# Optimization experiments

Hardware: AMD Instinct MI355X
Metric: run time of the kernel (lower is better)

The kernel has to match this reference:

```python
import jax, jax.numpy as jnp
import numpy as np

LAMBDA_SOFTMAX = 20.0  # opt.lambda_softmax
EPS = 1e-8
NEG = -1e30


def l2norm(x, axis):
    # torch l2norm: x / (sqrt(sum x^2) + eps)
    n = jnp.sqrt(jnp.sum(x * x, axis=axis, keepdims=True)) + EPS
    return x / n


def cosine(x1, x2, axis):
    # torch compute_similarity: sum(x1*x2)/clamp(|x1||x2|, min=eps)
    w12 = jnp.sum(x1 * x2, axis=axis)
    w1 = jnp.sqrt(jnp.sum(x1 * x1, axis=axis))
    w2 = jnp.sqrt(jnp.sum(x2 * x2, axis=axis))
    return w12 / jnp.maximum(w1 * w2, EPS)


def _focal_renorm(a, sourceL):
    # focal_equal: fattn = 1[a*S - sum(a) > 0], then renormalize fattn*a
    funcF = a * sourceL - jnp.sum(a, axis=-1, keepdims=True)
    fattn = jnp.where(funcF > 0, 1.0, 0.0)
    ta = fattn * a
    s = jnp.sum(ta, axis=-1, keepdims=True)
    return ta / jnp.where(s > 0, s, 1.0)


def compute_weiTexts(img_q, img_v, txt_k_all, txt_v_all, text_length):
    N, R, d = img_q.shape          # n_img, n_region, d
    Lw = txt_k_all.shape[1]        # max words
    qn_img = l2norm(img_q, -1)     # [N,R,d]
    mask_all = (jnp.arange(Lw)[None, :] < text_length[:, None])  # [T,Lw] bool

    def per_text(txt_k, txt_v, mask, n_word):
        # mask out padded words (torch slices [:n_word])
        m = mask.astype(txt_k.dtype)[:, None]        # [Lw,1]
        tk = l2norm(txt_k * m, -1)                   # [Lw,d], padded rows -> 0
        tv = txt_v * m                                # [Lw,d]

        # ---- i2t: query=img, context=text (sourceL = n_word) ----
        attn = jnp.einsum('ld,nrd->nlr', tk, qn_img)  # bmm(key_norm, queryT) [N,Lw,R]
        attn = jax.nn.leaky_relu(attn, 0.1)
        attn = l2norm(attn, 2)                        # over R
        attn = jnp.transpose(attn, (0, 2, 1))         # [N,R,Lw]
        logits = jnp.where(mask[None, None, :], attn * LAMBDA_SOFTMAX, NEG)
        a = jax.nn.softmax(logits, axis=-1)           # [N,R,Lw]
        a = _focal_renorm(a, n_word)
        wei_text = jnp.einsum('nrl,ld->nrd', a, tv)   # [N,R,d]
        wei_text = l2norm(wei_text, 2)
        i2t = jnp.mean(cosine(img_v, wei_text, 2), axis=1)  # [N]

        # ---- t2i: query=text, context=img (sourceL = R) ----
        attn2 = jnp.einsum('nrd,ld->nrl', qn_img, tk)  # bmm(key_norm, queryT) [N,R,Lw]
        attn2 = jax.nn.leaky_relu(attn2, 0.1)
        attn2 = l2norm(attn2, 2)                       # over Lw (padded cols are 0)
        attn2 = jnp.transpose(attn2, (0, 2, 1))        # [N,Lw,R]
        a2 = jax.nn.softmax(attn2 * LAMBDA_SOFTMAX, axis=-1)
        a2 = _focal_renorm(a2, float(R))
        wei_img = jnp.einsum('nlr,nrd->nld', a2, img_v)  # [N,Lw,d]
        wei_img = l2norm(wei_img, 2)
        cos2 = cosine(tv[None, :, :], wei_img, 2)        # [N,Lw]; padded rows -> 0
        t2i = jnp.sum(cos2 * mask.astype(cos2.dtype)[None, :], axis=1) / n_word
        return i2t, t2i

    n_word_f = text_length.astype(img_q.dtype)
    i2t_T, t2i_T = jax.vmap(per_text)(txt_k_all, txt_v_all, mask_all, n_word_f)
    # loop concatenated along dim 1 -> [n_img, n_txt]
    return i2t_T.T, t2i_T.T


def setup_inputs() -> dict:
    key = jax.random.key(0)
    k1, k2, k3, k4, k5 = jax.random.split(key, 5)
    N, T, R, Lw, d = 128, 128, 48, 64, 1024
    return {
        'local_img_query': jax.random.normal(k1, (N, R, d), dtype=jnp.float32),
        'local_img_value': jax.random.normal(k2, (N, R, d), dtype=jnp.float32),
        'local_text_key': jax.random.normal(k3, (T, Lw, d), dtype=jnp.float32),
        'local_text_value': jax.random.normal(k4, (T, Lw, d), dtype=jnp.float32),
        'text_length': jax.random.randint(k5, (T,), 16, Lw + 1, dtype=jnp.int32),
    }


def reference(local_img_query, local_img_value, local_text_key, local_text_value, text_length):
    return compute_weiTexts(local_img_query, local_img_value,
                            local_text_key, local_text_value, text_length)
```

## Files before the change

### kernel.cpp

```cpp
#include <hip/hip_runtime.h>

#define NIMG 128
#define NTXT 128
#define RDIM 48
#define LWRD 64
#define DDIM 1024
#define LAMB 20.0f
#define FEPS 1e-8f

#define WS_INVQ 0
#define WS_VN   6144
#define WS_INVK 12288
#define WS_TVN  20480
#define WS_H    28672
#define WS_VG   552960
#define WS_MID_BYTES 3391488ull
#define WS_HU   847872
#define WS_VGU  1372160
#define SP_TK   3334144
#define SP_TV   20111360
#define SP_Q    36888576
#define SP_V    49471488
#define WS_BIG_BYTES 124108800ull

typedef unsigned int u32;
typedef unsigned short u16;
typedef __attribute__((ext_vector_type(8))) short short8;
typedef __attribute__((ext_vector_type(4))) float f32x4;
typedef __attribute__((ext_vector_type(4))) u32 uintx4;
typedef __attribute__((ext_vector_type(2))) u32 uintx2;

#define MFMA(a,b,c) __builtin_amdgcn_mfma_f32_16x16x32_bf16(a,b,c,0,0,0)

__device__ __forceinline__ u32 f2bf(float x){
    u32 u = __float_as_uint(x);
    return (u + 0x7fffu + ((u >> 16) & 1u)) >> 16;
}
__device__ __forceinline__ float bf2f(u32 h){ return __uint_as_float(h << 16); }
__device__ __forceinline__ u32 packsplit(float x){
    u32 h = f2bf(x);
    u32 l = f2bf(x - bf2f(h));
    return h | (l << 16);
}
__device__ __forceinline__ void unpk(uintx4 a, uintx4 b, short8& hi, short8& lo){
    uintx4 h, l;
    h.x = (a.x & 0xffffu) | (a.y << 16);
    h.y = (a.z & 0xffffu) | (a.w << 16);
    h.z = (b.x & 0xffffu) | (b.y << 16);
    h.w = (b.z & 0xffffu) | (b.w << 16);
    l.x = (a.x >> 16) | (a.y & 0xffff0000u);
    l.y = (a.z >> 16) | (a.w & 0xffff0000u);
    l.z = (b.x >> 16) | (b.y & 0xffff0000u);
    l.w = (b.z >> 16) | (b.w & 0xffff0000u);
    hi = __builtin_bit_cast(short8, h);
    lo = __builtin_bit_cast(short8, l);
}

#define PSTR  40
#define PTKH  0
#define PTVH  2560
#define PQH   5120
#define PVH   8960
#define LOGAP 12800
__device__ __forceinline__ void split_store(short* stg, int idx, float4 x, float sc){
    float a0 = x.x*sc, a1 = x.y*sc, a2 = x.z*sc, a3 = x.w*sc;
    u32 h0=f2bf(a0), h1=f2bf(a1), h2=f2bf(a2), h3=f2bf(a3);
    u32 l0=f2bf(a0-bf2f(h0)), l1=f2bf(a1-bf2f(h1)), l2=f2bf(a2-bf2f(h2)), l3=f2bf(a3-bf2f(h3));
    uintx2 hv; hv.x = h0 | (h1<<16); hv.y = h2 | (h3<<16);
    uintx2 lv; lv.x = l0 | (l1<<16); lv.y = l2 | (l3<<16);
    *(uintx2*)(stg + idx)         = hv;
    *(uintx2*)(stg + idx + LOGAP) = lv;
}
__device__ __forceinline__ short8 frag_ld(const short* stg, int plane, int rb, int m16, int quad){
    return *(const short8*)(stg + plane + (rb + m16) * PSTR + quad * 8);
}

__global__ __launch_bounds__(256, 2)
void prep_norms(const float* __restrict__ imq, const float* __restrict__ imv,
                const float* __restrict__ txk, const float* __restrict__ txv,
                float* __restrict__ ws) {
    int vid = blockIdx.x * 4 + (threadIdx.x >> 6);
    int lane = threadIdx.x & 63;
    const float* src;
    if (vid < 6144)       src = imq + (size_t)vid * 1024;
    else if (vid < 12288) src = imv + (size_t)(vid - 6144) * 1024;
    else if (vid < 20480) src = txk + (size_t)(vid - 12288) * 1024;
    else                  src = txv + (size_t)(vid - 20480) * 1024;
    const float4* s4 = (const float4*)src;
    float acc = 0.f;
#pragma unroll
    for (int j = 0; j < 4; ++j) {
        float4 v = s4[lane + 64 * j];
        acc += v.x * v.x + v.y * v.y + v.z * v.z + v.w * v.w;
    }
#pragma unroll
    for (int off = 32; off; off >>= 1) acc += __shfl_down(acc, off, 64);
    if (lane == 0) {
        float nrm = sqrtf(acc);
        if (vid < 6144)       ws[vid] = 1.f / (nrm + FEPS);
        else if (vid < 12288) ws[vid] = nrm;
        else if (vid < 20480) ws[vid] = 1.f / (nrm + FEPS);
        else                  ws[vid] = nrm;
    }
}

__global__ __launch_bounds__(256, 2)
void split_kernel(const float* __restrict__ imq, const float* __restrict__ imv,
                  const float* __restrict__ txk, const float* __restrict__ txv,
                  const int* __restrict__ tlen, const float* __restrict__ wsf,
// ... 22 lines not shown
        sc = (ten == 2) ? wsf[WS_INVQ + slab * 48 + row] : 1.f;
        dst = (size_t)(ten == 2 ? SP_Q : SP_V) + (size_t)slab * 98304
            + kc * 1536 + row * 32 + ks * 8;
        psz = 49152;
    }
    float4 x0 = *(const float4*)src;
    float4 x1 = *(const float4*)(src + 4);
    float v[8] = {x0.x, x0.y, x0.z, x0.w, x1.x, x1.y, x1.z, x1.w};
    short8 hv, lv;
#pragma unroll
    for (int i = 0; i < 8; ++i) {
        float a = v[i] * sc;
        u32 h = f2bf(a);
        hv[i] = (short)h;
        lv[i] = (short)f2bf(a - bf2f(h));
    }
    *(short8*)(wss + dst) = hv;
    *(short8*)(wss + dst + psz) = lv;
}

template <int TS>
__device__ __forceinline__ void gram_body(const float* __restrict__ src,
                                          float* __restrict__ dstf,
                                          u32* __restrict__ dstu,
                                          int mode, int nw, float* sT){
    const int NR = TS * 16;
    int ar = threadIdx.x >> 4, ac = threadIdx.x & 15;
    float acc[TS][TS];
#pragma unroll
    for (int i = 0; i < TS; ++i)
#pragma unroll
        for (int j = 0; j < TS; ++j) acc[i][j] = 0.f;
    for (int kc = 0; kc < 8; ++kc) {
        int k0 = kc * 128;
        for (int jid = threadIdx.x; jid < NR * 32; jid += 256) {
            int row = jid >> 5, c4 = jid & 31;
            float4 x = *(const float4*)(src + row * 1024 + k0 + c4 * 4);
            float sc = (row < nw) ? 1.f : 0.f;
            x.x *= sc; x.y *= sc; x.z *= sc; x.w *= sc;
            *(float4*)&sT[row * 132 + c4 * 4] = x;
        }
        __syncthreads();
#pragma unroll 4
        for (int k4 = 0; k4 < 32; ++k4) {
            float4 av[TS], bv[TS];
#pragma unroll
            for (int i = 0; i < TS; ++i) av[i] = *(const float4*)&sT[(TS*ar + i) * 132 + k4 * 4];
#pragma unroll
            for (int j = 0; j < TS; ++j) bv[j] = *(const float4*)&sT[(TS*ac + j) * 132 + k4 * 4];
#pragma unroll
            for (int i = 0; i < TS; ++i)
#pragma unroll
                for (int j = 0; j < TS; ++j)
                    acc[i][j] += av[i].x*bv[j].x + av[i].y*bv[j].y + av[i].z*bv[j].z + av[i].w*bv[j].w;
        }
        __syncthreads();
    }
#pragma unroll
    for (int i = 0; i < TS; ++i)
#pragma unroll
        for (int j = 0; j < TS; ++j) {
            int idx = (TS*ar + i) * NR + TS*ac + j;
            if (mode) dstu[idx] = packsplit(acc[i][j]);
            else      dstf[idx] = acc[i][j];
        }
}

__global__ __launch_bounds__(256, 2)
void gram_kernel(const float* __restrict__ txv, const float* __restrict__ imv,
                 const int* __restrict__ tlen, float* __restrict__ ws, int mode){
    __shared__ __align__(16) float sT[64 * 132];
    int b = blockIdx.x;
    u32* wsu = (u32*)ws;
    if (b < 128) {
        gram_body<4>(txv + (size_t)b * 65536, ws + WS_H + (size_t)b * 4096,
                     wsu + WS_HU + (size_t)b * 4096, mode, tlen[b], sT);
    } else {
        int n = b - 128;
        gram_body<3>(imv + (size_t)n * 49152, ws + WS_VG + (size_t)n * 2304,
                     wsu + WS_VGU + (size_t)n * 2304, mode, 48, sT);
    }
}

struct AFr { short8 kh[2], kl[2], th[2], tl[2]; };

__device__ __forceinline__ void load_af(AFr& A, const short* tkh, const short* tkl,
                                        const short* tvh, const short* tvl,
                                        int off, int r0, int r1){
    A.kh[0] = *(const short8*)(tkh + off + r0);
    A.kh[1] = *(const short8*)(tkh + off + r1);
    A.kl[0] = *(const short8*)(tkl + off + r0);
    A.kl[1] = *(const short8*)(tkl + off + r1);
    A.th[0] = *(const short8*)(tvh + off + r0);
    A.th[1] = *(const short8*)(tvh + off + r1);
    A.tl[0] = *(const short8*)(tvl + off + r0);
    A.tl[1] = *(const short8*)(tvl + off + r1);
}

__device__ __forceinline__ void mfma_step(const AFr& A, const short* stg,
                                          int nl, int m16, int quad,
                                          f32x4 (&accS)[2][3], f32x4 (&accG)[2][3]){
#pragma unroll
    for (int j = 0; j < 3; ++j) {
        int o = (nl * 48 + 16 * j + m16) * 40 + quad * 8;
        short8 bqh = *(const short8*)(stg + o);
        short8 bql = *(const short8*)(stg + 3840 + o);
        short8 bvh = *(const short8*)(stg + 7680 + o);
        short8 bvl = *(const short8*)(stg + 11520 + o);
#pragma unroll
        for (int i = 0; i < 2; ++i) {
            accS[i][j] = MFMA(A.kh[i], bqh, accS[i][j]);
            accS[i][j] = MFMA(A.kh[i], bql, accS[i][j]);
            accS[i][j] = MFMA(A.kl[i], bqh, accS[i][j]);
            accG[i][j] = MFMA(A.th[i], bvh, accG[i][j]);
            accG[i][j] = MFMA(A.th[i], bvl, accG[i][j]);
            accG[i][j] = MFMA(A.tl[i], bvh, accG[i][j]);
        }
    }
}

__global__ __launch_bounds__(256, 2)
void loss_mfma2(const int* __restrict__ tlen, const float* __restrict__ ws,
                float* __restrict__ out) {
    const int npair = blockIdx.x;
    const int t     = blockIdx.y;
    const int n0    = npair * 2;
    const int tid   = threadIdx.x;
    const int lane  = tid & 63;
    const int w     = tid >> 6;
    const int nl    = w >> 1;
    const int hh    = w & 1;
    const int quad  = lane >> 4;
    const int m16   = lane & 15;

    __shared__ __align__(16) float Sm[19776];
    short* stg   = (short*)Sm;
    u32*   A1w   = (u32*)Sm;
    u32*   A2w   = ((u32*)Sm) + 6528;
    float* P     = Sm + 12672;
    u32*   HVw   = (u32*)(Sm + 12672);
    float* sNl   = Sm + 19104;
    float* sNr   = Sm + 19232;
    float* sD1   = Sm + 19328;
    float* sS1   = Sm + 19424;
    float* sD2   = Sm + 19520;
    float* sS2   = Sm + 19648;

    const int nw = tlen[t];
    const float nwf = (float)nw;
    const short* wss = (const short*)ws;
    const u32*   wsu = (const u32*)ws;

    const short* bsrc[6]; int bdst[6];
#pragma unroll
    for (int it = 0; it < 6; ++it) {
        int jid = tid + 256 * it;
        int p = jid / 384; int rr = jid - p * 384;
        int row = rr >> 2, ks = rr & 3;
        int img = row >= 48; int grow = row - 48 * img;
        bsrc[it] = wss + (p < 2 ? SP_Q : SP_V) + (size_t)(n0 + img) * 98304
                 + (size_t)(p & 1) * 49152 + grow * 32 + ks * 8;
        bdst[it] = p * 3840 + row * 40 + ks * 8;
    }

    const short* tkh = wss + SP_TK + (size_t)t * 131072;
    const short* tkl = tkh + 65536;
    const short* tvh = wss + SP_TV + (size_t)t * 131072;
    const short* tvl = tvh + 65536;
    const int ar0 = (32 * hh + m16) * 32 + quad * 8;
    const int ar1 = ar0 + 512;

    f32x4 accS[2][3], accG[2][3];
    f32x4 zf = {0.f, 0.f, 0.f, 0.f};
#pragma unroll
    for (int i = 0; i < 2; ++i)
#pragma unroll
        for (int j = 0; j < 3; ++j) { accS[i][j] = zf; accG[i][j] = zf; }

    short8 bj[6];
#pragma unroll
    for (int it = 0; it < 6; ++it) bj[it] = *(const short8*)(bsrc[it]);
    AFr Ae, Ao;
    load_af(Ae, tkh, tkl, tvh, tvl, 0, ar0, ar1);

    for (int kc2 = 0; kc2 < 16; ++kc2) {
        const int kc = kc2 * 2;
        {
#pragma unroll
            for (int it = 0; it < 6; ++it) *(short8*)(stg + bdst[it]) = bj[it];
            __syncthreads();
            int bo = (kc + 1) * 1536;
#pragma unroll
            for (int it = 0; it < 6; ++it) bj[it] = *(const short8*)(bsrc[it] + bo);
            load_af(Ao, tkh, tkl, tvh, tvl, (kc + 1) * 2048, ar0, ar1);
            mfma_step(Ae, stg, nl, m16, quad, accS, accG);
            __syncthreads();
        }
        {
#pragma unroll
            for (int it = 0; it < 6; ++it) *(short8*)(stg + bdst[it]) = bj[it];
            __syncthreads();
            if (kc2 < 15) {
                int bo = (kc + 2) * 1536;
#pragma unroll
                for (int it = 0; it < 6; ++it) bj[it] = *(const short8*)(bsrc[it] + bo);
                load_af(Ae, tkh, tkl, tvh, tvl, (kc + 2) * 2048, ar0, ar1);
            }
            mfma_step(Ao, stg, nl, m16, quad, accS, accG);
            __syncthreads();
        }
    }

#pragma unroll
    for (int i = 0; i < 2; ++i)
#pragma unroll
        for (int j = 0; j < 3; ++j)
#pragma unroll
            for (int v = 0; v < 4; ++v) {
                int l = 32 * hh + 16 * i + quad * 4 + v;
                int r = 16 * j + m16;
                float x = accS[i][j][v];
                P[nl * 3136 + l * 49 + r] = (x > 0.f) ? x : 0.1f * x;
            }
    __syncthreads();

    if (tid < 128) {
        int n = tid >> 6, l = tid & 63;
        float s = 0.f;
#pragma unroll 4
        for (int r = 0; r < 48; ++r) { float x = P[n*3136 + l*49 + r]; s += x * x; }
        sNl[n * 64 + l] = sqrtf(s) + FEPS;
    } else if (tid < 224) {
        int i = tid - 128; int n = i >= 48; int r = i - 48 * n;
        float s = 0.f;
#pragma unroll 4
        for (int l = 0; l < 64; ++l) { float x = P[n*3136 + l*49 + r]; s += x * x; }
        sNr[n * 48 + r] = sqrtf(s) + FEPS;
    } else {
        for (int k = tid - 224; k < 448; k += 32) sD1[k] = 0.f;
    }
    __syncthreads();

    if (tid < 128) {
        int n = tid >> 6, l = tid & 63;
        u32* row = A2w + n * 3072 + l * 48;
        if (l < nw) {
            float a[48]; float mx = -1e30f;
            const float* Pr = P + n * 3136 + l * 49;
#pragma unroll
            for (int r = 0; r < 48; ++r) {
                float x = LAMB * Pr[r] / sNr[n * 48 + r];
                a[r] = x; mx = fmaxf(mx, x);
            }
            float se = 0.f;
#pragma unroll
            for (int r = 0; r < 48; ++r) { float e = __expf(a[r] - mx); a[r] = e; se += e; }
            float suma = 0.f;
#pragma unroll
            for (int r = 0; r < 48; ++r) { float x = a[r] / se; a[r] = x; suma += x; }
            float s2 = 0.f;
#pragma unroll
            for (int r = 0; r < 48; ++r) if (a[r] * 48.f - suma > 0.f) s2 += a[r];
            float ri = (s2 > 0.f) ? 1.f / s2 : 1.f;
#pragma unroll
            for (int r = 0; r < 48; ++r) {
                float x = (a[r] * 48.f - suma > 0.f) ? a[r] * ri : 0.f;
                row[r] = packsplit(x);
            }
        } else {
#pragma unroll
            for (int r = 0; r < 48; ++r) row[r] = 0u;
        }
    } else if (tid < 224) {
        int i = tid - 128; int n = i >= 48; int r = i - 48 * n;
        float a[64]; float mx = -1e30f;
#pragma unroll
        for (int l = 0; l < 64; ++l) {
            float x = (l < nw) ? (LAMB * P[n*3136 + l*49 + r] / sNl[n * 64 + l]) : -1e30f;
            a[l] = x; mx = fmaxf(mx, x);
        }
        float se = 0.f;
#pragma unroll
        for (int l = 0; l < 64; ++l) { float e = __expf(a[l] - mx); a[l] = e; se += e; }
        float suma = 0.f;
#pragma unroll
        for (int l = 0; l < 64; ++l) { float x = a[l] / se; a[l] = x; suma += x; }
        float s2 = 0.f;
#pragma unroll
        for (int l = 0; l < 64; ++l) if (a[l] * nwf - suma > 0.f) s2 += a[l];
        float ri = (s2 > 0.f) ? 1.f / s2 : 1.f;
        u32* row = A1w + n * 3264 + r * 68;
#pragma unroll
        for (int l = 0; l < 64; ++l) {
            float x = (a[l] * nwf - suma > 0.f) ? a[l] * ri : 0.f;
            row[l] = packsplit(x);
        }
    }
    __syncthreads();

    {
        const u32* Hg = wsu + WS_HU + (size_t)t * 4096;
        for (int jid = tid; jid < 1024; jid += 256) {
            int row = jid >> 4, c = jid & 15;
            *(uintx4*)&HVw[row * 68 + c * 4] = *(const uintx4*)&Hg[row * 64 + c * 4];
        }
    }
    __syncthreads();

    f32x4 accY[2][3];
    f32x4 zf2 = {0.f, 0.f, 0.f, 0.f};
#pragma unroll
    for (int i = 0; i < 2; ++i)
#pragma unroll
        for (int j = 0; j < 3; ++j) accY[i][j] = zf2;
#pragma unroll
    for (int ks = 0; ks < 2; ++ks) {
        int kb = ks * 32 + quad * 8;
        short8 Ah[2], Al[2];
#pragma unroll
        for (int i = 0; i < 2; ++i) {
            int row = 32 * hh + 16 * i + m16;
            uintx4 wa = *(const uintx4*)&HVw[row * 68 + kb];
            uintx4 wb = *(const uintx4*)&HVw[row * 68 + kb + 4];
            unpk(wa, wb, Ah[i], Al[i]);
        }
        short8 Bh[3], Bl[3];
#pragma unroll
        for (int j = 0; j < 3; ++j) {
            int base = nl * 3264 + (16 * j + m16) * 68 + kb;
            uintx4 wa = *(const uintx4*)&A1w[base];
            uintx4 wb = *(const uintx4*)&A1w[base + 4];
            unpk(wa, wb, Bh[j], Bl[j]);
        }
#pragma unroll
        for (int i = 0; i < 2; ++i)
#pragma unroll
            for (int j = 0; j < 3; ++j) {
                accY[i][j] = MFMA(Ah[i], Bh[j], accY[i][j]);
                accY[i][j] = MFMA(Ah[i], Bl[j], accY[i][j]);
                accY[i][j] = MFMA(Al[i], Bh[j], accY[i][j]);
            }
    }
    {
        float td[3] = {0.f, 0.f, 0.f}, ts[3] = {0.f, 0.f, 0.f};
#pragma unroll
        for (int i = 0; i < 2; ++i)
#pragma unroll
            for (int v = 0; v < 4; ++v) {
                int l = 32 * hh + 16 * i + quad * 4 + v;
#pragma unroll
                for (int j = 0; j < 3; ++j) {
                    u32 wv = A1w[nl * 3264 + (16 * j + m16) * 68 + l];
                    float av = bf2f(wv & 0xffffu) + bf2f(wv >> 16);
                    td[j] += av * accG[i][j][v];
                    ts[j] += av * accY[i][j][v];
                }
            }
#pragma unroll
        for (int j = 0; j < 3; ++j) {
            float d = td[j]; d += __shfl_xor(d, 16, 64); d += __shfl_xor(d, 32, 64);
            float s = ts[j]; s += __shfl_xor(s, 16, 64); s += __shfl_xor(s, 32, 64);
            if (quad == 0) {
                atomicAdd(&sD1[nl * 48 + 16 * j + m16], d);
                atomicAdd(&sS1[nl * 48 + 16 * j + m16], s);
            }
        }
    }
    __syncthreads();

    {
        const u32* Vgg = wsu + WS_VGU + (size_t)n0 * 2304;
        for (int jid = tid; jid < 1152; jid += 256) {
            int img = jid >= 576; int j2 = jid - 576 * img;
            int row = j2 / 12, c = j2 - row * 12;
            *(uintx4*)&HVw[img * 2496 + row * 52 + c * 4] =
                *(const uintx4*)&Vgg[(size_t)img * 2304 + row * 48 + c * 4];
        }
    }
    __syncthreads();

    f32x4 accY2[3][2];
#pragma unroll
    for (int i = 0; i < 3; ++i)
#pragma unroll
        for (int j = 0; j < 2; ++j) accY2[i][j] = zf2;
    const u32* VgW = HVw + nl * 2496;
#pragma unroll
    for (int ks = 0; ks < 2; ++ks) {
        const bool dead = (ks == 1) && (quad >= 2);
        const int kb = (ks == 0) ? quad * 8 : 32 + (quad & 1) * 8;
        short8 Ah2[3], Al2[3];
#pragma unroll
        for (int i = 0; i < 3; ++i) {
            uintx4 wa = {0,0,0,0}, wb = {0,0,0,0};
            if (!dead) {
                int row = 16 * i + m16;
                wa = *(const uintx4*)&VgW[row * 52 + kb];
                wb = *(const uintx4*)&VgW[row * 52 + kb + 4];
            }
            unpk(wa, wb, Ah2[i], Al2[i]);
        }
        short8 Bh2[2], Bl2[2];
#pragma unroll
        for (int j = 0; j < 2; ++j) {
            uintx4 wa = {0,0,0,0}, wb = {0,0,0,0};
            if (!dead) {
                int l = 32 * hh + 16 * j + m16;
                wa = *(const uintx4*)&A2w[nl * 3072 + l * 48 + kb];
                wb = *(const uintx4*)&A2w[nl * 3072 + l * 48 + kb + 4];
            }
            unpk(wa, wb, Bh2[j], Bl2[j]);
        }
#pragma unroll
        for (int i = 0; i < 3; ++i)
#pragma unroll
            for (int j = 0; j < 2; ++j) {
                accY2[i][j] = MFMA(Ah2[i], Bh2[j], accY2[i][j]);
                accY2[i][j] = MFMA(Ah2[i], Bl2[j], accY2[i][j]);
                accY2[i][j] = MFMA(Al2[i], Bh2[j], accY2[i][j]);
            }
    }
    {
        float u[2] = {0.f, 0.f};
#pragma unroll
        for (int i = 0; i < 3; ++i)
#pragma unroll
            for (int v = 0; v < 4; ++v) {
                int r = 16 * i + quad * 4 + v;
#pragma unroll
                for (int j = 0; j < 2; ++j) {
                    int l = 32 * hh + 16 * j + m16;
                    u32 wv = A2w[nl * 3072 + l * 48 + r];
                    float av = bf2f(wv & 0xffffu) + bf2f(wv >> 16);
                    u[j] += av * accY2[i][j][v];
                }
            }
#pragma unroll
        for (int j = 0; j < 2; ++j) {
            float s = u[j]; s += __shfl_xor(s, 16, 64); s += __shfl_xor(s, 32, 64);
            if (quad == 0) sS2[nl * 64 + 32 * hh + 16 * j + m16] = s;
        }
        float ud[2][4];
#pragma unroll
        for (int i = 0; i < 2; ++i)
#pragma unroll
            for (int v = 0; v < 4; ++v) ud[i][v] = 0.f;
#pragma unroll
        for (int i = 0; i < 2; ++i)
#pragma unroll
            for (int v = 0; v < 4; ++v) {
                int l = 32 * hh + 16 * i + quad * 4 + v;
#pragma unroll
                for (int j = 0; j < 3; ++j) {
                    u32 wv = A2w[nl * 3072 + l * 48 + (16 * j + m16)];
                    float av = bf2f(wv & 0xffffu) + bf2f(wv >> 16);
                    ud[i][v] += av * accG[i][j][v];
                }
            }
#pragma unroll
        for (int i = 0; i < 2; ++i)
#pragma unroll
            for (int v = 0; v < 4; ++v) {
                float d = ud[i][v];
                d += __shfl_xor(d, 1, 64); d += __shfl_xor(d, 2, 64);
                d += __shfl_xor(d, 4, 64); d += __shfl_xor(d, 8, 64);
                if (m16 == 0) sD2[nl * 64 + 32 * hh + 16 * i + quad * 4 + v] = d;
            }
    }
    __syncthreads();

    if (tid < 96) {
        int n = tid >= 48; int r = tid - 48 * n;
        float wn = sqrtf(sS1[n * 48 + r]);
        float dh = sD1[n * 48 + r] / (wn + FEPS);
        float nh = wn / (wn + FEPS);
        float vn = ws[WS_VN + (n0 + n) * 48 + r];
        sD1[n * 48 + r] = dh / fmaxf(vn * nh, FEPS);
    } else if (tid >= 128) {
        int i = tid - 128; int n = i >> 6, l = i & 63;
        if (l < nw) {
            float wn = sqrtf(sS2[n * 64 + l]);
            float dh = sD2[n * 64 + l] / (wn + FEPS);
            float nh = wn / (wn + FEPS);
            float tn = ws[WS_TVN + t * 64 + l];
            sD2[n * 64 + l] = dh / fmaxf(tn * nh, FEPS);
        }
    }
    __syncthreads();
    if (tid < 2) {
        float s = 0.f;
        for (int r = 0; r < 48; ++r) s += sD1[tid * 48 + r];
        out[(size_t)(n0 + tid) * NTXT + t] = s / 48.f;
    } else if (tid == 64 || tid == 65) {
        int n = tid - 64;
        float s = 0.f;
        for (int l = 0; l < nw; ++l) s += sD2[n * 64 + l];
        out[(size_t)(NIMG * NTXT) + (size_t)(n0 + n) * NTXT + t] = s / nwf;
    }
}

__global__ __launch_bounds__(256, 2)
void loss_mfma(const float* __restrict__ imq, const float* __restrict__ imv,
               const float* __restrict__ txk, const float* __restrict__ txv,
               const int* __restrict__ tlen, const float* __restrict__ ws,
               float* __restrict__ out) {
    const int npair = blockIdx.x;
    const int t     = blockIdx.y;
    const int n0    = npair * 2;
    const int tid   = threadIdx.x;
    const int lane  = tid & 63;
    const int w     = tid >> 6;
    const int nl    = w >> 1;
    const int hh    = w & 1;
    const int quad  = lane >> 4;
    const int m16   = lane & 15;

    __shared__ __align__(16) float Sm[19904];
    short* stage = (short*)Sm;
    u32*   A1w   = (u32*)Sm;
    u32*   A2w   = ((u32*)Sm) + 6528;
    float* P     = Sm + 12800;
    u32*   HVw   = (u32*)(Sm + 12800);
    float* sInvK = Sm + 19072;
    float* sInvQ = sInvK + 64;
    float* sNl   = sInvQ + 96;
    float* sNr   = sNl + 128;
    float* sD1   = sNr + 96;
    float* sS1   = sD1 + 96;
    float* sD2   = sS1 + 96;
    float* sS2   = sD2 + 128;

    const int nw = tlen[t];
    const float nwf = (float)nw;
    if (tid < 64) sInvK[tid] = ws[WS_INVK + t * 64 + tid];
    else if (tid < 160) {
        int i = tid - 64; int nn = i >= 48; int r = i - 48 * nn;
        sInvQ[i] = ws[WS_INVQ + (n0 + nn) * 48 + r];
    }
    __syncthreads();

    const float* tkb = txk + (size_t)t * 65536;
    const float* tvb = txv + (size_t)t * 65536;
    const float* qb0 = imq + (size_t)n0 * 49152;
    const float* vb0 = imv + (size_t)n0 * 49152;

    const float* sp[10]; int di[10]; float scl[10];
#pragma unroll
    for (int it = 0; it < 10; ++it) {
        int jid = tid + 256 * it;
        const float* s; int plane; int row, c4; float sc;
        if (it < 2) {
            row = jid >> 3; c4 = jid & 7;
            s = tkb + row * 1024 + c4 * 4;
            sc = (row < nw) ? sInvK[row] : 0.f;
            plane = PTKH;
        } else if (it < 4) {
            int j2 = jid - 512; row = j2 >> 3; c4 = j2 & 7;
            s = tvb + row * 1024 + c4 * 4;
            sc = (row < nw) ? 1.f : 0.f;
            plane = PTVH;
        } else if (it < 7) {
            int j2 = jid - 1024; row = j2 >> 3; c4 = j2 & 7;
            s = qb0 + row * 1024 + c4 * 4;
            sc = sInvQ[row];
            plane = PQH;
        } else {
            int j2 = jid - 1792; row = j2 >> 3; c4 = j2 & 7;
            s = vb0 + row * 1024 + c4 * 4;
            sc = 1.f;
            plane = PVH;
        }
        sp[it] = s; di[it] = plane + row * PSTR + c4 * 4; scl[it] = sc;
    }

    f32x4 accS[2][3], accG[2][3];
    f32x4 zf = {0.f, 0.f, 0.f, 0.f};
#pragma unroll
    for (int i = 0; i < 2; ++i)
#pragma unroll
        for (int j = 0; j < 3; ++j) { accS[i][j] = zf; accG[i][j] = zf; }
// ... 272 lines not shown
                }
            }
#pragma unroll
        for (int j = 0; j < 2; ++j) {
            float s = u[j]; s += __shfl_xor(s, 16, 64); s += __shfl_xor(s, 32, 64);
            if (quad == 0) sS2[nl * 64 + 32 * hh + 16 * j + m16] = s;
        }
        float ud[2][4];
#pragma unroll
        for (int i = 0; i < 2; ++i)
#pragma unroll
            for (int v = 0; v < 4; ++v) ud[i][v] = 0.f;
#pragma unroll
        for (int i = 0; i < 2; ++i)
#pragma unroll
            for (int v = 0; v < 4; ++v) {
                int l = 32 * hh + 16 * i + quad * 4 + v;
#pragma unroll
                for (int j = 0; j < 3; ++j) {
                    u32 wv = A2w[nl * 3072 + l * 48 + (16 * j + m16)];
                    float av = bf2f(wv & 0xffffu) + bf2f(wv >> 16);
                    ud[i][v] += av * accG[i][j][v];
                }
            }
#pragma unroll
        for (int i = 0; i < 2; ++i)
#pragma unroll
            for (int v = 0; v < 4; ++v) {
                float d = ud[i][v];
                d += __shfl_xor(d, 1, 64); d += __shfl_xor(d, 2, 64);
                d += __shfl_xor(d, 4, 64); d += __shfl_xor(d, 8, 64);
                if (m16 == 0) sD2[nl * 64 + 32 * hh + 16 * i + quad * 4 + v] = d;
            }
    }
    __syncthreads();

    if (tid < 96) {
        int n = tid >= 48; int r = tid - 48 * n;
        float wn = sqrtf(sS1[n * 48 + r]);
        float dh = sD1[n * 48 + r] / (wn + FEPS);
        float nh = wn / (wn + FEPS);
        float vn = ws[WS_VN + (n0 + n) * 48 + r];
        sD1[n * 48 + r] = dh / fmaxf(vn * nh, FEPS);
    } else if (tid >= 128) {
        int i = tid - 128; int n = i >> 6, l = i & 63;
        if (l < nw) {
            float wn = sqrtf(sS2[n * 64 + l]);
            float dh = sD2[n * 64 + l] / (wn + FEPS);
            float nh = wn / (wn + FEPS);
            float tn = ws[WS_TVN + t * 64 + l];
            sD2[n * 64 + l] = dh / fmaxf(tn * nh, FEPS);
        }
    }
    __syncthreads();
    if (tid < 2) {
        float s = 0.f;
        for (int r = 0; r < 48; ++r) s += sD1[tid * 48 + r];
        out[(size_t)(n0 + tid) * NTXT + t] = s / 48.f;
    } else if (tid == 64 || tid == 65) {
        int n = tid - 64;
        float s = 0.f;
        for (int l = 0; l < nw; ++l) s += sD2[n * 64 + l];
        out[(size_t)(NIMG * NTXT) + (size_t)(n0 + n) * NTXT + t] = s / nwf;
    }
}

extern "C" void kernel_launch(void* const* d_in, const int* in_sizes, int n_in,
                              void* d_out, int out_size, void* d_ws, size_t ws_size,
                              hipStream_t stream) {
    (void)in_sizes; (void)n_in; (void)out_size;
    const float* imq = (const float*)d_in[0];
    const float* imv = (const float*)d_in[1];
    const float* txk = (const float*)d_in[2];
    const float* txv = (const float*)d_in[3];
    const int*   tln = (const int*)d_in[4];
    float* out = (float*)d_out;
    float* ws  = (float*)d_ws;

    prep_norms<<<7168, 256, 0, stream>>>(imq, imv, txk, txv, ws);
    if (ws_size >= WS_BIG_BYTES) {
        split_kernel<<<dim3(4096, 4), 256, 0, stream>>>(imq, imv, txk, txv, tln,
                                                        ws, (short*)d_ws);
        gram_kernel<<<256, 256, 0, stream>>>(txv, imv, tln, ws, 1);
        dim3 grid(64, 128);
        loss_mfma2<<<grid, 256, 0, stream>>>(tln, ws, out);
    } else {
        gram_kernel<<<256, 256, 0, stream>>>(txv, imv, tln, ws, 0);
        dim3 grid(64, 128);
        loss_mfma<<<grid, 256, 0, stream>>>(imq, imv, txk, txv, tln, ws, out);
    }
}
```

Baseline: 1.123 ms.

## Process one image per block in loss kernel to raise occupancy

Replaces the two-images-per-block loss kernel with a one-image-per-block version on a 128x128 grid. Each wave now owns 16 text rows instead of 32, which shrinks accumulators and shared memory, and launch bounds are raised to 4 blocks per CU. The text Gram and image Gram matrices are read straight from global memory instead of being staged through shared memory, which removes those copies and a few barriers. In exchange, each text's split key/value fragments are loaded twice as often across blocks, raising global/L2 traffic.

```diff
diff --git a/kernel.cpp b/kernel.cpp
--- a/kernel.cpp
+++ b/kernel.cpp
@@ -24,7 +24,6 @@
 #define WS_BIG_BYTES 124108800ull
 
 typedef unsigned int u32;
-typedef unsigned short u16;
 typedef __attribute__((ext_vector_type(8))) short short8;
 typedef __attribute__((ext_vector_type(4))) float f32x4;
 typedef __attribute__((ext_vector_type(4))) u32 uintx4;
@@ -213,174 +212,155 @@
     }
 }
 
-struct AFr { short8 kh[2], kl[2], th[2], tl[2]; };
-
-__device__ __forceinline__ void load_af(AFr& A, const short* tkh, const short* tkl,
-                                        const short* tvh, const short* tvl,
-                                        int off, int r0, int r1){
-    A.kh[0] = *(const short8*)(tkh + off + r0);
-    A.kh[1] = *(const short8*)(tkh + off + r1);
-    A.kl[0] = *(const short8*)(tkl + off + r0);
-    A.kl[1] = *(const short8*)(tkl + off + r1);
-    A.th[0] = *(const short8*)(tvh + off + r0);
-    A.th[1] = *(const short8*)(tvh + off + r1);
-    A.tl[0] = *(const short8*)(tvl + off + r0);
-    A.tl[1] = *(const short8*)(tvl + off + r1);
-}
-
-__device__ __forceinline__ void mfma_step(const AFr& A, const short* stg,
-                                          int nl, int m16, int quad,
-                                          f32x4 (&accS)[2][3], f32x4 (&accG)[2][3]){
-#pragma unroll
-    for (int j = 0; j < 3; ++j) {
-        int o = (nl * 48 + 16 * j + m16) * 40 + quad * 8;
-        short8 bqh = *(const short8*)(stg + o);
-        short8 bql = *(const short8*)(stg + 3840 + o);
-        short8 bvh = *(const short8*)(stg + 7680 + o);
-        short8 bvl = *(const short8*)(stg + 11520 + o);
-#pragma unroll
-        for (int i = 0; i < 2; ++i) {
-            accS[i][j] = MFMA(A.kh[i], bqh, accS[i][j]);
-            accS[i][j] = MFMA(A.kh[i], bql, accS[i][j]);
-            accS[i][j] = MFMA(A.kl[i], bqh, accS[i][j]);
-            accG[i][j] = MFMA(A.th[i], bvh, accG[i][j]);
-            accG[i][j] = MFMA(A.th[i], bvl, accG[i][j]);
-            accG[i][j] = MFMA(A.tl[i], bvh, accG[i][j]);
-        }
-    }
-}
-
-__global__ __launch_bounds__(256, 2)
-void loss_mfma2(const int* __restrict__ tlen, const float* __restrict__ ws,
+__global__ __launch_bounds__(256, 4)
+void loss_mfma3(const int* __restrict__ tlen, const float* __restrict__ ws,
                 float* __restrict__ out) {
-    const int npair = blockIdx.x;
-    const int t     = blockIdx.y;
-    const int n0    = npair * 2;
-    const int tid   = threadIdx.x;
-    const int lane  = tid & 63;
-    const int w     = tid >> 6;
-    const int nl    = w >> 1;
-    const int hh    = w & 1;
-    const int quad  = lane >> 4;
-    const int m16   = lane & 15;
-
-    __shared__ __align__(16) float Sm[19776];
-    short* stg   = (short*)Sm;
-    u32*   A1w   = (u32*)Sm;
-    u32*   A2w   = ((u32*)Sm) + 6528;
-    float* P     = Sm + 12672;
-    u32*   HVw   = (u32*)(Sm + 12672);
-    float* sNl   = Sm + 19104;
-    float* sNr   = Sm + 19232;
-    float* sD1   = Sm + 19328;
-    float* sS1   = Sm + 19424;
-    float* sD2   = Sm + 19520;
-    float* sS2   = Sm + 19648;
+    const int n    = blockIdx.x;
+    const int t    = blockIdx.y;
+    const int tid  = threadIdx.x;
+    const int lane = tid & 63;
+    const int w    = tid >> 6;
+    const int quad = lane >> 4;
+    const int m16  = lane & 15;
+
+    __shared__ __align__(16) float Sm[10064];
+    u32*   A1w = (u32*)Sm;
+    u32*   A2w = ((u32*)Sm) + 3264;
+    short* stg = (short*)Sm;
+    float* P   = Sm + 6592;
+    float* sNl = Sm + 9728;
+    float* sNr = Sm + 9792;
+    float* sD1 = Sm + 9840;
+    float* sS1 = Sm + 9888;
+    float* sD2 = Sm + 9936;
+    float* sS2 = Sm + 10000;
 
     const int nw = tlen[t];
     const float nwf = (float)nw;
     const short* wss = (const short*)ws;
     const u32*   wsu = (const u32*)ws;
 
-    const short* bsrc[6]; int bdst[6];
-#pragma unroll
-    for (int it = 0; it < 6; ++it) {
+    const short* bsrc[3]; int bdst[3];
+#pragma unroll
+    for (int it = 0; it < 3; ++it) {
         int jid = tid + 256 * it;
-        int p = jid / 384; int rr = jid - p * 384;
+        int p = jid / 192; int rr = jid - p * 192;
         int row = rr >> 2, ks = rr & 3;
-        int img = row >= 48; int grow = row - 48 * img;
-        bsrc[it] = wss + (p < 2 ? SP_Q : SP_V) + (size_t)(n0 + img) * 98304
-                 + (size_t)(p & 1) * 49152 + grow * 32 + ks * 8;
-        bdst[it] = p * 3840 + row * 40 + ks * 8;
+        bsrc[it] = wss + (p < 2 ? SP_Q : SP_V) + (size_t)n * 98304
+                 + (size_t)(p & 1) * 49152 + row * 32 + ks * 8;
+        bdst[it] = p * 1920 + row * 40 + ks * 8;
     }
 
     const short* tkh = wss + SP_TK + (size_t)t * 131072;
     const short* tkl = tkh + 65536;
     const short* tvh = wss + SP_TV + (size_t)t * 131072;
     const short* tvl = tvh + 65536;
-    const int ar0 = (32 * hh + m16) * 32 + quad * 8;
-    const int ar1 = ar0 + 512;
-
-    f32x4 accS[2][3], accG[2][3];
+    const int ar = (16 * w + m16) * 32 + quad * 8;
+
+    f32x4 accS[3], accG[3];
     f32x4 zf = {0.f, 0.f, 0.f, 0.f};
 #pragma unroll
-    for (int i = 0; i < 2; ++i)
-#pragma unroll
-        for (int j = 0; j < 3; ++j) { accS[i][j] = zf; accG[i][j] = zf; }
-
-    short8 bj[6];
-#pragma unroll
-    for (int it = 0; it < 6; ++it) bj[it] = *(const short8*)(bsrc[it]);
-    AFr Ae, Ao;
-    load_af(Ae, tkh, tkl, tvh, tvl, 0, ar0, ar1);
+    for (int j = 0; j < 3; ++j) { accS[j] = zf; accG[j] = zf; }
+
+    short8 bj[3];
+#pragma unroll
+    for (int it = 0; it < 3; ++it) bj[it] = *(const short8*)(bsrc[it]);
+    short8 kh0, kl0, th0, tl0, kh1, kl1, th1, tl1;
+    kh0 = *(const short8*)(tkh + ar); kl0 = *(const short8*)(tkl + ar);
+    th0 = *(const short8*)(tvh + ar); tl0 = *(const short8*)(tvl + ar);
 
     for (int kc2 = 0; kc2 < 16; ++kc2) {
         const int kc = kc2 * 2;
         {
 #pragma unroll
-            for (int it = 0; it < 6; ++it) *(short8*)(stg + bdst[it]) = bj[it];
+            for (int it = 0; it < 3; ++it) *(short8*)(stg + bdst[it]) = bj[it];
             __syncthreads();
-            int bo = (kc + 1) * 1536;
-#pragma unroll
-            for (int it = 0; it < 6; ++it) bj[it] = *(const short8*)(bsrc[it] + bo);
-            load_af(Ao, tkh, tkl, tvh, tvl, (kc + 1) * 2048, ar0, ar1);
-            mfma_step(Ae, stg, nl, m16, quad, accS, accG);
+            int bo = (kc + 1) * 1536, ao = (kc + 1) * 2048 + ar;
+#pragma unroll
+            for (int it = 0; it < 3; ++it) bj[it] = *(const short8*)(bsrc[it] + bo);
+            kh1 = *(const short8*)(tkh + ao); kl1 = *(const short8*)(tkl + ao);
+            th1 = *(const short8*)(tvh + ao); tl1 = *(const short8*)(tvl + ao);
+#pragma unroll
+            for (int j = 0; j < 3; ++j) {
+                int o = (16 * j + m16) * 40 + quad * 8;
+                short8 bqh = *(const short8*)(stg + o);
+                short8 bql = *(const short8*)(stg + 1920 + o);
+                short8 bvh = *(const short8*)(stg + 3840 + o);
+                short8 bvl = *(const short8*)(stg + 5760 + o);
+                accS[j] = MFMA(kh0, bqh, accS[j]);
+                accS[j] = MFMA(kh0, bql, accS[j]);
+                accS[j] = MFMA(kl0, bqh, accS[j]);
+                accG[j] = MFMA(th0, bvh, accG[j]);
+                accG[j] = MFMA(th0, bvl, accG[j]);
+                accG[j] = MFMA(tl0, bvh, accG[j]);
+            }
             __syncthreads();
         }
         {
 #pragma unroll
-            for (int it = 0; it < 6; ++it) *(short8*)(stg + bdst[it]) = bj[it];
+            for (int it = 0; it < 3; ++it) *(short8*)(stg + bdst[it]) = bj[it];
             __syncthreads();
             if (kc2 < 15) {
-                int bo = (kc + 2) * 1536;
-#pragma unroll
-                for (int it = 0; it < 6; ++it) bj[it] = *(const short8*)(bsrc[it] + bo);
-                load_af(Ae, tkh, tkl, tvh, tvl, (kc + 2) * 2048, ar0, ar1);
-            }
-            mfma_step(Ao, stg, nl, m16, quad, accS, accG);
+                int bo = (kc + 2) * 1536, ao = (kc + 2) * 2048 + ar;
+#pragma unroll
+                for (int it = 0; it < 3; ++it) bj[it] = *(const short8*)(bsrc[it] + bo);
+                kh0 = *(const short8*)(tkh + ao); kl0 = *(const short8*)(tkl + ao);
+                th0 = *(const short8*)(tvh + ao); tl0 = *(const short8*)(tvl + ao);
+            }
+#pragma unroll
+            for (int j = 0; j < 3; ++j) {
+                int o = (16 * j + m16) * 40 + quad * 8;
+                short8 bqh = *(const short8*)(stg + o);
+                short8 bql = *(const short8*)(stg + 1920 + o);
+                short8 bvh = *(const short8*)(stg + 3840 + o);
+                short8 bvl = *(const short8*)(stg + 5760 + o);
+                accS[j] = MFMA(kh1, bqh, accS[j]);
+                accS[j] = MFMA(kh1, bql, accS[j]);
+                accS[j] = MFMA(kl1, bqh, accS[j]);
+                accG[j] = MFMA(th1, bvh, accG[j]);
+                accG[j] = MFMA(th1, bvl, accG[j]);
+                accG[j] = MFMA(tl1, bvh, accG[j]);
+            }
             __syncthreads();
         }
     }
 
 #pragma unroll
-    for (int i = 0; i < 2; ++i)
-#pragma unroll
-        for (int j = 0; j < 3; ++j)
-#pragma unroll
-            for (int v = 0; v < 4; ++v) {
-                int l = 32 * hh + 16 * i + quad * 4 + v;
-                int r = 16 * j + m16;
-                float x = accS[i][j][v];
-                P[nl * 3136 + l * 49 + r] = (x > 0.f) ? x : 0.1f * x;
-            }
-    __syncthreads();
-
-    if (tid < 128) {
-        int n = tid >> 6, l = tid & 63;
+    for (int j = 0; j < 3; ++j)
+#pragma unroll
+        for (int v = 0; v < 4; ++v) {
+            int l = 16 * w + quad * 4 + v;
+            float x = accS[j][v];
+            P[l * 49 + 16 * j + m16] = (x > 0.f) ? x : 0.1f * x;
+        }
+    __syncthreads();
+
+    if (tid < 64) {
         float s = 0.f;
 #pragma unroll 4
-        for (int r = 0; r < 48; ++r) { float x = P[n*3136 + l*49 + r]; s += x * x; }
-        sNl[n * 64 + l] = sqrtf(s) + FEPS;
-    } else if (tid < 224) {
-        int i = tid - 128; int n = i >= 48; int r = i - 48 * n;
+        for (int r = 0; r < 48; ++r) { float x = P[tid * 49 + r]; s += x * x; }
+        sNl[tid] = sqrtf(s) + FEPS;
+    } else if (tid < 112) {
+        int r = tid - 64;
         float s = 0.f;
 #pragma unroll 4
-        for (int l = 0; l < 64; ++l) { float x = P[n*3136 + l*49 + r]; s += x * x; }
-        sNr[n * 48 + r] = sqrtf(s) + FEPS;
-    } else {
-        for (int k = tid - 224; k < 448; k += 32) sD1[k] = 0.f;
-    }
-    __syncthreads();
-
-    if (tid < 128) {
-        int n = tid >> 6, l = tid & 63;
-        u32* row = A2w + n * 3072 + l * 48;
+        for (int l = 0; l < 64; ++l) { float x = P[l * 49 + r]; s += x * x; }
+        sNr[r] = sqrtf(s) + FEPS;
+    } else if (tid < 208) {
+        int k = tid - 112;
+        if (k < 48) sD1[k] = 0.f; else sS1[k - 48] = 0.f;
+    }
+    __syncthreads();
+
+    if (tid < 64) {
+        int l = tid;
+        u32* row = A2w + l * 52;
         if (l < nw) {
             float a[48]; float mx = -1e30f;
-            const float* Pr = P + n * 3136 + l * 49;
+            const float* Pr = P + l * 49;
 #pragma unroll
             for (int r = 0; r < 48; ++r) {
-                float x = LAMB * Pr[r] / sNr[n * 48 + r];
+                float x = LAMB * Pr[r] / sNr[r];
                 a[r] = x; mx = fmaxf(mx, x);
             }
             float se = 0.f;
@@ -402,12 +382,12 @@
 #pragma unroll
             for (int r = 0; r < 48; ++r) row[r] = 0u;
         }
-    } else if (tid < 224) {
-        int i = tid - 128; int n = i >= 48; int r = i - 48 * n;
+    } else if (tid < 112) {
+        int r = tid - 64;
         float a[64]; float mx = -1e30f;
 #pragma unroll
         for (int l = 0; l < 64; ++l) {
-            float x = (l < nw) ? (LAMB * P[n*3136 + l*49 + r] / sNl[n * 64 + l]) : -1e30f;
+            float x = (l < nw) ? (LAMB * P[l * 49 + r] / sNl[l]) : -1e30f;
             a[l] = x; mx = fmaxf(mx, x);
         }
         float se = 0.f;
@@ -420,7 +400,7 @@
 #pragma unroll
         for (int l = 0; l < 64; ++l) if (a[l] * nwf - suma > 0.f) s2 += a[l];
         float ri = (s2 > 0.f) ? 1.f / s2 : 1.f;
-        u32* row = A1w + n * 3264 + r * 68;
+        u32* row = A1w + r * 68;
 #pragma unroll
         for (int l = 0; l < 64; ++l) {
             float x = (a[l] * nwf - suma > 0.f) ? a[l] * ri : 0.f;
@@ -429,204 +409,147 @@
     }
     __syncthreads();
 
-    {
-        const u32* Hg = wsu + WS_HU + (size_t)t * 4096;
-        for (int jid = tid; jid < 1024; jid += 256) {
-            int row = jid >> 4, c = jid & 15;
-            *(uintx4*)&HVw[row * 68 + c * 4] = *(const uintx4*)&Hg[row * 64 + c * 4];
-        }
-    }
-    __syncthreads();
-
-    f32x4 accY[2][3];
-    f32x4 zf2 = {0.f, 0.f, 0.f, 0.f};
-#pragma unroll
-    for (int i = 0; i < 2; ++i)
-#pragma unroll
-        for (int j = 0; j < 3; ++j) accY[i][j] = zf2;
+    f32x4 accY[3];
+#pragma unroll
+    for (int j = 0; j < 3; ++j) accY[j] = zf;
+    const u32* Hg = wsu + WS_HU + (size_t)t * 4096 + (16 * w + m16) * 64;
 #pragma unroll
     for (int ks = 0; ks < 2; ++ks) {
         int kb = ks * 32 + quad * 8;
-        short8 Ah[2], Al[2];
-#pragma unroll
-        for (int i = 0; i < 2; ++i) {
-            int row = 32 * hh + 16 * i + m16;
-            uintx4 wa = *(const uintx4*)&HVw[row * 68 + kb];
-            uintx4 wb = *(const uintx4*)&HVw[row * 68 + kb + 4];
-            unpk(wa, wb, Ah[i], Al[i]);
-        }
-        short8 Bh[3], Bl[3];
+        short8 Ah, Al;
+        {
+            uintx4 wa = *(const uintx4*)&Hg[kb];
+            uintx4 wb = *(const uintx4*)&Hg[kb + 4];
+            unpk(wa, wb, Ah, Al);
+        }
 #pragma unroll
         for (int j = 0; j < 3; ++j) {
-            int base = nl * 3264 + (16 * j + m16) * 68 + kb;
+            int base = (16 * j + m16) * 68 + kb;
             uintx4 wa = *(const uintx4*)&A1w[base];
             uintx4 wb = *(const uintx4*)&A1w[base + 4];
-            unpk(wa, wb, Bh[j], Bl[j]);
-        }
-#pragma unroll
-        for (int i = 0; i < 2; ++i)
-#pragma unroll
-            for (int j = 0; j < 3; ++j) {
-                accY[i][j] = MFMA(Ah[i], Bh[j], accY[i][j]);
-                accY[i][j] = MFMA(Ah[i], Bl[j], accY[i][j]);
-                accY[i][j] = MFMA(Al[i], Bh[j], accY[i][j]);
-            }
+            short8 Bh, Bl;
+            unpk(wa, wb, Bh, Bl);
+            accY[j] = MFMA(Ah, Bh, accY[j]);
+            accY[j] = MFMA(Ah, Bl, accY[j]);
+            accY[j] = MFMA(Al, Bh, accY[j]);
+        }
     }
     {
         float td[3] = {0.f, 0.f, 0.f}, ts[3] = {0.f, 0.f, 0.f};
 #pragma unroll
-        for (int i = 0; i < 2; ++i)
-#pragma unroll
-            for (int v = 0; v < 4; ++v) {
-                int l = 32 * hh + 16 * i + quad * 4 + v;
-#pragma unroll
-                for (int j = 0; j < 3; ++j) {
-                    u32 wv = A1w[nl * 3264 + (16 * j + m16) * 68 + l];
-                    float av = bf2f(wv & 0xffffu) + bf2f(wv >> 16);
-                    td[j] += av * accG[i][j][v];
-                    ts[j] += av * accY[i][j][v];
-                }
-            }
+        for (int v = 0; v < 4; ++v) {
+            int l = 16 * w + quad * 4 + v;
+#pragma unroll
+            for (int j = 0; j < 3; ++j) {
+                u32 wv = A1w[(16 * j + m16) * 68 + l];
+                float av = bf2f(wv & 0xffffu) + bf2f(wv >> 16);
+                td[j] += av * accG[j][v];
+                ts[j] += av * accY[j][v];
+            }
+        }
 #pragma unroll
         for (int j = 0; j < 3; ++j) {
             float d = td[j]; d += __shfl_xor(d, 16, 64); d += __shfl_xor(d, 32, 64);
             float s = ts[j]; s += __shfl_xor(s, 16, 64); s += __shfl_xor(s, 32, 64);
             if (quad == 0) {
-                atomicAdd(&sD1[nl * 48 + 16 * j + m16], d);
-                atomicAdd(&sS1[nl * 48 + 16 * j + m16], s);
-            }
-        }
-    }
-    __syncthreads();
-
-    {
-        const u32* Vgg = wsu + WS_VGU + (size_t)n0 * 2304;
-        for (int jid = tid; jid < 1152; jid += 256) {
-            int img = jid >= 576; int j2 = jid - 576 * img;
-            int row = j2 / 12, c = j2 - row * 12;
-            *(uintx4*)&HVw[img * 2496 + row * 52 + c * 4] =
-                *(const uintx4*)&Vgg[(size_t)img * 2304 + row * 48 + c * 4];
-        }
-    }
-    __syncthreads();
-
-    f32x4 accY2[3][2];
-#pragma unroll
-    for (int i = 0; i < 3; ++i)
-#pragma unroll
-        for (int j = 0; j < 2; ++j) accY2[i][j] = zf2;
-    const u32* VgW = HVw + nl * 2496;
+                atomicAdd(&sD1[16 * j + m16], d);
+                atomicAdd(&sS1[16 * j + m16], s);
+            }
+        }
+    }
+
+    f32x4 accY2[3];
+#pragma unroll
+    for (int i = 0; i < 3; ++i) accY2[i] = zf;
+    const u32* Vgg = wsu + WS_VGU + (size_t)n * 2304;
 #pragma unroll
     for (int ks = 0; ks < 2; ++ks) {
         const bool dead = (ks == 1) && (quad >= 2);
         const int kb = (ks == 0) ? quad * 8 : 32 + (quad & 1) * 8;
-        short8 Ah2[3], Al2[3];
+        short8 Bh2, Bl2;
+        {
+            uintx4 wa = {0,0,0,0}, wb = {0,0,0,0};
+            if (!dead) {
+                int base = (16 * w + m16) * 52 + kb;
+                wa = *(const uintx4*)&A2w[base];
+                wb = *(const uintx4*)&A2w[base + 4];
+            }
+            unpk(wa, wb, Bh2, Bl2);
+        }
 #pragma unroll
         for (int i = 0; i < 3; ++i) {
             uintx4 wa = {0,0,0,0}, wb = {0,0,0,0};
             if (!dead) {
-                int row = 16 * i + m16;
-                wa = *(const uintx4*)&VgW[row * 52 + kb];
-                wb = *(const uintx4*)&VgW[row * 52 + kb + 4];
-            }
-            unpk(wa, wb, Ah2[i], Al2[i]);
-        }
-        short8 Bh2[2], Bl2[2];
-#pragma unroll
-        for (int j = 0; j < 2; ++j) {
-            uintx4 wa = {0,0,0,0}, wb = {0,0,0,0};
-            if (!dead) {
-                int l = 32 * hh + 16 * j + m16;
-                wa = *(const uintx4*)&A2w[nl * 3072 + l * 48 + kb];
-                wb = *(const uintx4*)&A2w[nl * 3072 + l * 48 + kb + 4];
-            }
-            unpk(wa, wb, Bh2[j], Bl2[j]);
-        }
-#pragma unroll
-        for (int i = 0; i < 3; ++i)
-#pragma unroll
-            for (int j = 0; j < 2; ++j) {
-                accY2[i][j] = MFMA(Ah2[i], Bh2[j], accY2[i][j]);
-                accY2[i][j] = MFMA(Ah2[i], Bl2[j], accY2[i][j]);
-                accY2[i][j] = MFMA(Al2[i], Bh2[j], accY2[i][j]);
-            }
+                wa = *(const uintx4*)&Vgg[(16 * i + m16) * 48 + kb];
+                wb = *(const uintx4*)&Vgg[(16 * i + m16) * 48 + kb + 4];
+            }
+            short8 Ah2, Al2;
+            unpk(wa, wb, Ah2, Al2);
+            accY2[i] = MFMA(Ah2, Bh2, accY2[i]);
+            accY2[i] = MFMA(Ah2, Bl2, accY2[i]);
+            accY2[i] = MFMA(Al2, Bh2, accY2[i]);
+        }
     }
     {
-        float u[2] = {0.f, 0.f};
+        float u = 0.f;
 #pragma unroll
         for (int i = 0; i < 3; ++i)
 #pragma unroll
             for (int v = 0; v < 4; ++v) {
                 int r = 16 * i + quad * 4 + v;
-#pragma unroll
-                for (int j = 0; j < 2; ++j) {
-                    int l = 32 * hh + 16 * j + m16;
-                    u32 wv = A2w[nl * 3072 + l * 48 + r];
-                    float av = bf2f(wv & 0xffffu) + bf2f(wv >> 16);
-                    u[j] += av * accY2[i][j][v];
-                }
-            }
-#pragma unroll
-        for (int j = 0; j < 2; ++j) {
-            float s = u[j]; s += __shfl_xor(s, 16, 64); s += __shfl_xor(s, 32, 64);
-            if (quad == 0) sS2[nl * 64 + 32 * hh + 16 * j + m16] = s;
-        }
-        float ud[2][4];
-#pragma unroll
-        for (int i = 0; i < 2; ++i)
-#pragma unroll
-            for (int v = 0; v < 4; ++v) ud[i][v] = 0.f;
-#pragma unroll
-        for (int i = 0; i < 2; ++i)
-#pragma unroll
-            for (int v = 0; v < 4; ++v) {
-                int l = 32 * hh + 16 * i + quad * 4 + v;
-#pragma unroll
-                for (int j = 0; j < 3; ++j) {
-                    u32 wv = A2w[nl * 3072 + l * 48 + (16 * j + m16)];
-                    float av = bf2f(wv & 0xffffu) + bf2f(wv >> 16);
-                    ud[i][v] += av * accG[i][j][v];
-                }
-            }
-#pragma unroll
-        for (int i = 0; i < 2; ++i)
-#pragma unroll
-            for (int v = 0; v < 4; ++v) {
-                float d = ud[i][v];
-                d += __shfl_xor(d, 1, 64); d += __shfl_xor(d, 2, 64);
-                d += __shfl_xor(d, 4, 64); d += __shfl_xor(d, 8, 64);
-                if (m16 == 0) sD2[nl * 64 + 32 * hh + 16 * i + quad * 4 + v] = d;
-            }
-    }
-    __syncthreads();
-
-    if (tid < 96) {
-        int n = tid >= 48; int r = tid - 48 * n;
-        float wn = sqrtf(sS1[n * 48 + r]);
-        float dh = sD1[n * 48 + r] / (wn + FEPS);
+                u32 wv = A2w[(16 * w + m16) * 52 + r];
+                float av = bf2f(wv & 0xffffu) + bf2f(wv >> 16);
+                u += av * accY2[i][v];
+            }
+        u += __shfl_xor(u, 16, 64); u += __shfl_xor(u, 32, 64);
+        if (quad == 0) sS2[16 * w + m16] = u;
+        float ud[4] = {0.f, 0.f, 0.f, 0.f};
+#pragma unroll
+        for (int v = 0; v < 4; ++v) {
+            int l = 16 * w + quad * 4 + v;
+#pragma unroll
+            for (int j = 0; j < 3; ++j) {
+                u32 wv = A2w[l * 52 + 16 * j + m16];
+                float av = bf2f(wv & 0xffffu) + bf2f(wv >> 16);
+                ud[v] += av * accG[j][v];
+            }
+        }
+#pragma unroll
+        for (int v = 0; v < 4; ++v) {
+            float d = ud[v];
+            d += __shfl_xor(d, 1, 64); d += __shfl_xor(d, 2, 64);
+            d += __shfl_xor(d, 4, 64); d += __shfl_xor(d, 8, 64);
+            if (m16 == 0) sD2[16 * w + quad * 4 + v] = d;
+        }
+    }
+    __syncthreads();
+
+    if (tid < 48) {
+        int r = tid;
+        float wn = sqrtf(sS1[r]);
+        float dh = sD1[r] / (wn + FEPS);
         float nh = wn / (wn + FEPS);
-        float vn = ws[WS_VN + (n0 + n) * 48 + r];
-        sD1[n * 48 + r] = dh / fmaxf(vn * nh, FEPS);
-    } else if (tid >= 128) {
-        int i = tid - 128; int n = i >> 6, l = i & 63;
+        float vn = ws[WS_VN + n * 48 + r];
+        sD1[r] = dh / fmaxf(vn * nh, FEPS);
+    } else if (tid >= 64 && tid < 128) {
+        int l = tid - 64;
         if (l < nw) {
-            float wn = sqrtf(sS2[n * 64 + l]);
-            float dh = sD2[n * 64 + l] / (wn + FEPS);
+            float wn = sqrtf(sS2[l]);
+            float dh = sD2[l] / (wn + FEPS);
             float nh = wn / (wn + FEPS);
             float tn = ws[WS_TVN + t * 64 + l];
-            sD2[n * 64 + l] = dh / fmaxf(tn * nh, FEPS);
-        }
-    }
-    __syncthreads();
-    if (tid < 2) {
+            sD2[l] = dh / fmaxf(tn * nh, FEPS);
+        }
+    }
+    __syncthreads();
+    if (tid == 0) {
         float s = 0.f;
-        for (int r = 0; r < 48; ++r) s += sD1[tid * 48 + r];
-        out[(size_t)(n0 + tid) * NTXT + t] = s / 48.f;
-    } else if (tid == 64 || tid == 65) {
-        int n = tid - 64;
+        for (int r = 0; r < 48; ++r) s += sD1[r];
+        out[(size_t)n * NTXT + t] = s / 48.f;
+    } else if (tid == 64) {
         float s = 0.f;
-        for (int l = 0; l < nw; ++l) s += sD2[n * 64 + l];
-        out[(size_t)(NIMG * NTXT) + (size_t)(n0 + n) * NTXT + t] = s / nwf;
+        for (int l = 0; l < nw; ++l) s += sD2[l];
+        out[(size_t)(NIMG * NTXT) + (size_t)n * NTXT + t] = s / nwf;
     }
 }
 
@@ -1065,8 +988,8 @@
         split_kernel<<<dim3(4096, 4), 256, 0, stream>>>(imq, imv, txk, txv, tln,
                                                         ws, (short*)d_ws);
         gram_kernel<<<256, 256, 0, stream>>>(txv, imv, tln, ws, 1);
-        dim3 grid(64, 128);
-        loss_mfma2<<<grid, 256, 0, stream>>>(tln, ws, out);
+        dim3 grid(NIMG, NTXT);
+        loss_mfma3<<<grid, 256, 0, stream>>>(tln, ws, out);
     } else {
         gram_kernel<<<256, 256, 0, stream>>>(txv, imv, tln, ws, 0);
         dim3 grid(64, 128);
```

Result: faster. 1.063 ms (-5.4%).
